# Kernel optimization log

Hardware: AMD Instinct MI355X
Metric: run time of the kernel (lower is better)

## Reference

```python
import jax, jax.numpy as jnp
import numpy as np

N_TRIPLES = 100_000    # number of (head, rel, attr) triples
TOTAL_CHARS = 1_600_000  # total characters across all attribute strings (~16/triple)
CHAR_VOCAB = 10_000
N_ENT = 100_000
D = 128                # embedding dim shared by char and entity tables


def setup_inputs() -> dict:
    key = jax.random.key(0)
    k1, k2, k3, k4, k5 = jax.random.split(key, 5)
    char_embeddings = jax.random.normal(k1, (CHAR_VOCAB, D), dtype=jnp.float32)
    entity_embeddings = jax.random.normal(k2, (N_ENT, D), dtype=jnp.float32)
    head_ids = jax.random.randint(k3, (N_TRIPLES,), 0, N_ENT, dtype=jnp.int32)
    char_ids = jax.random.randint(k4, (TOTAL_CHARS,), 0, CHAR_VOCAB, dtype=jnp.int32)
    # sorted segment ids emulate the per-triple ragged grouping (offsets form)
    segment_ids = jnp.sort(jax.random.randint(k5, (TOTAL_CHARS,), 0, N_TRIPLES, dtype=jnp.int32))
    return {
        "char_embeddings": char_embeddings,
        "entity_embeddings": entity_embeddings,
        "head_ids": head_ids,
        "char_ids": char_ids,
        "segment_ids": segment_ids,
    }


def reference(char_embeddings, entity_embeddings, head_ids, char_ids, segment_ids):
    n = head_ids.shape[0]
    # ragged embedding-bag: gather char rows, sum within each triple's segment
    t = jax.ops.segment_sum(char_embeddings[char_ids], segment_ids, num_segments=n)  # [N, D]
    h = entity_embeddings[head_ids]  # [N, D]
    # torch.norm with no dim = global Frobenius norm (faithful to original)
    h = h / jnp.linalg.norm(h)
    t = t / jnp.linalg.norm(t)
    return jnp.sum(1.0 - jnp.sum(h * t, axis=1))
```

## Files before the change

### kernel.cpp

```cpp
#include <hip/hip_runtime.h>

#define DIM   128
#define HALF  64
#define CPT   256
#define TAIL  64
#define WPB   4
#define NHID  (CPT + 1)

__global__ __launch_bounds__(256) void fused_kernel(
    const float* __restrict__ char_emb,
    const float* __restrict__ ent,
    const int* __restrict__ head_ids,
    const int* __restrict__ char_ids,
    const int* __restrict__ seg_ids,
    float* __restrict__ pb,
    int total_chars, int n_triples, int hh_per_block)
{
    __shared__ __align__(16) int s_off[WPB][CPT + TAIL];
    __shared__ int s_sid[WPB][CPT + TAIL];
    __shared__ int s_hid[WPB][NHID];
    __shared__ float r_scr[3][WPB];

    const int tid  = threadIdx.x;
    const int lane = tid & 63;
    const int wid  = tid >> 6;
    const int colb = lane << 2;

    float ht = 0.f, tt = 0.f, hh = 0.f;

    const int slice = blockIdx.x & 1;
    const int sco   = slice << 8;
    const int chunk = (blockIdx.x >> 1) * WPB + wid;
    const int start = chunk * CPT;
    const int len   = min(CPT, total_chars - start);
    const int sl    = min(CPT + TAIL, total_chars - start);
    const char* cb  = (const char*)char_emb;
    const float* ee = ent + slice * HALF + lane;

    for (int c = lane; c < sl; c += 64) {
        s_off[wid][c] = (char_ids[start + c] << 9) + sco;
        s_sid[wid][c] = seg_ids[start + c];
    }

    unsigned long long mk[4] = {0ull, 0ull, 0ull, 0ull};
    int nb = 0;
    if (len == CPT) {
#pragma unroll
        for (int grp = 0; grp < 4; ++grp) {
            const int c = start + grp * 64 + lane;
            const int s1 = seg_ids[c];
            const int s0 = (c > 0) ? seg_ids[c - 1] : s1;
            const bool bnd = (c == 0) || (s1 != s0);
            const unsigned long long m = __ballot(bnd);
            if (bnd) {
                const int ord = nb + __builtin_amdgcn_mbcnt_hi(
                    (unsigned)(m >> 32),
                    __builtin_amdgcn_mbcnt_lo((unsigned)m, 0));
                s_hid[wid][ord] = head_ids[s0];
            }
            mk[grp] = m;
            nb += __popcll(m);
        }
        if (lane == 0)
            s_hid[wid][nb] = head_ids[seg_ids[start + CPT - 1]];
    }
    __syncthreads();

    if (len == CPT) {
        const int fin = seg_ids[start + CPT - 1];
        float acc = 0.f;
        bool live = false;
        int f = 0;
        const int h0 = s_hid[wid][0];
        const int h1 = s_hid[wid][min(1, nb)];
        int hidn     = s_hid[wid][min(2, nb)];
        float hv  = ee[(size_t)(unsigned)h0 * DIM];
        float hvn = ee[(size_t)(unsigned)h1 * DIM];
        float vA[16], vB[16];

#define PF(BUF, B) { \
    _Pragma("unroll") \
    for (int q = 0; q < 4; ++q) { \
        const int4 o4 = *(const int4*)&s_off[wid][(B) * 16 + q * 4]; \
        BUF[q * 4 + 0] = *(const float*)(cb + (size_t)(unsigned)(o4.x + colb)); \
        BUF[q * 4 + 1] = *(const float*)(cb + (size_t)(unsigned)(o4.y + colb)); \
        BUF[q * 4 + 2] = *(const float*)(cb + (size_t)(unsigned)(o4.z + colb)); \
        BUF[q * 4 + 3] = *(const float*)(cb + (size_t)(unsigned)(o4.w + colb)); \
    } }

#define CS(BUF, B) { \
    _Pragma("unroll") \
    for (int j = 0; j < 16; ++j) { \
        if (mk[(B) >> 2] & (1ull << (((B) & 3) * 16 + j))) {   \
            if (live) { ht = fmaf(hv, acc, ht); tt = fmaf(acc, acc, tt); } \
            live = true; acc = 0.f; \
            hv = hvn;                                     \
            hvn = ee[(size_t)(unsigned)hidn * DIM]; \
            ++f; \
            hidn = s_hid[wid][min(f + 2, nb)]; \
        } \
        acc += BUF[j]; \
    } }

        PF(vA, 0)
#pragma unroll
        for (int B = 0; B < 16; ++B) {
            if (B + 1 < 16) { if (B & 1) { PF(vA, B + 1) } else { PF(vB, B + 1) } }
            if (B & 1) { CS(vB, B) } else { CS(vA, B) }
        }
#undef PF
#undef CS

        if (live) {
            int e = CPT;
            bool ended = false;
            while (e < sl) {
                const int idx = e + lane;
                const bool differ = (idx < sl) && (s_sid[wid][idx] != fin);
                const unsigned long long bm = __ballot(differ);
                const int run = bm ? (__ffsll((long long)bm) - 1)
                                   : min(64, sl - e);
                for (int j = 0; j < run; j += 4) {
                    const int mm2 = min(4, run - j);
                    float vv[4];
#pragma unroll
                    for (int k = 0; k < 4; ++k) {
                        if (k < mm2)
                            vv[k] = *(const float*)(cb +
                                (size_t)(unsigned)(s_off[wid][e + j + k] + colb));
                    }
                    for (int k = 0; k < mm2; ++k) acc += vv[k];
                }
                e += run;
                if (bm) { ended = true; break; }
            }
            if (!ended && start + sl < total_chars) {
                int gg = start + sl;
                while (gg < total_chars && seg_ids[gg] == fin) {
                    acc += *(const float*)(cb +
                        (size_t)(unsigned)((char_ids[gg] << 9) + sco + colb));
                    ++gg;
                }
            }
            ht = fmaf(hv, acc, ht);
            tt = fmaf(acc, acc, tt);
        }
    } else if (len > 0) {
        const float* cembF = char_emb + slice * HALF + lane;
        int p = 0;
        if (start > 0) {
            const int prev = seg_ids[start - 1];
            while (p < len && seg_ids[start + p] == prev) ++p;
        }
        if (p < len) {
            int cur = seg_ids[start + p];
            float acc = 0.f;
            float hv = ee[(size_t)(unsigned)head_ids[cur] * DIM];
            for (int c = p; c < len; ++c) {
                const int sid = seg_ids[start + c];
                if (sid != cur) {
                    ht += hv * acc; tt += acc * acc;
                    acc = 0.f; cur = sid;
                    hv = ee[(size_t)(unsigned)head_ids[cur] * DIM];
                }
                acc += cembF[(size_t)(unsigned)char_ids[start + c] * DIM];
            }
            int gg = start + len;
            while (gg < total_chars && seg_ids[gg] == cur) {
                acc += cembF[(size_t)(unsigned)char_ids[gg] * DIM];
                ++gg;
            }
            ht += hv * acc; tt += acc * acc;
        }
    }

    {
        const float4* e4 = (const float4*)ent;
        const long base = (long)blockIdx.x * hh_per_block * 32;
        const long lim  = (long)n_triples * 32;
        for (int s = tid; s < hh_per_block * 32; s += 256) {
            const long f2 = base + s;
            if (f2 < lim) {
                const int row = (int)(f2 >> 5);
                const int hid = head_ids[row];
                const float4 v = e4[(size_t)hid * 32 + (int)(f2 & 31)];
                hh += v.x * v.x + v.y * v.y + v.z * v.z + v.w * v.w;
            }
        }
    }

#pragma unroll
    for (int off = 32; off > 0; off >>= 1) {
        ht += __shfl_down(ht, off);
        tt += __shfl_down(tt, off);
        hh += __shfl_down(hh, off);
    }
    if (lane == 0) { r_scr[0][wid] = ht; r_scr[1][wid] = tt; r_scr[2][wid] = hh; }
    __syncthreads();
    if (tid == 0) {
        float a = 0.f, b = 0.f, c = 0.f;
#pragma unroll
        for (int w = 0; w < WPB; ++w) {
            a += r_scr[0][w]; b += r_scr[1][w]; c += r_scr[2][w];
        }
        pb[blockIdx.x * 3 + 0] = a;
        pb[blockIdx.x * 3 + 1] = b;
        pb[blockIdx.x * 3 + 2] = c;
    }
}

__global__ __launch_bounds__(256) void reduce_kernel(
    const float* __restrict__ pb, int nb, float* __restrict__ out,
    int n_triples)
{
    double ht = 0.0, tt = 0.0, hh = 0.0;
    for (int i = threadIdx.x; i < nb; i += 256) {
        ht += (double)pb[i * 3 + 0];
        tt += (double)pb[i * 3 + 1];
        hh += (double)pb[i * 3 + 2];
    }
#pragma unroll
    for (int off = 32; off > 0; off >>= 1) {
        ht += __shfl_down(ht, off);
        tt += __shfl_down(tt, off);
        hh += __shfl_down(hh, off);
    }
    __shared__ double sd[3][4];
    const int wid = threadIdx.x >> 6;
    if ((threadIdx.x & 63) == 0) { sd[0][wid] = ht; sd[1][wid] = tt; sd[2][wid] = hh; }
    __syncthreads();
    if (threadIdx.x == 0) {
        double a = 0.0, b = 0.0, c = 0.0;
        for (int w = 0; w < 4; ++w) { a += sd[0][w]; b += sd[1][w]; c += sd[2][w]; }
        out[0] = (float)((double)n_triples - a / sqrt(c * b));
    }
}

extern "C" void kernel_launch(void* const* d_in, const int* in_sizes, int n_in,
                              void* d_out, int out_size, void* d_ws, size_t ws_size,
                              hipStream_t stream)
{
    const float* char_emb = (const float*)d_in[0];
    const float* ent_emb  = (const float*)d_in[1];
    const int* head_ids   = (const int*)d_in[2];
    const int* char_ids   = (const int*)d_in[3];
    const int* seg_ids    = (const int*)d_in[4];
    const int n_triples   = in_sizes[2];
    const int total_chars = in_sizes[3];

    const int n_chunks = (total_chars + CPT - 1) / CPT;
    const int bps = (n_chunks + WPB - 1) / WPB;
    const int nsb = 2 * bps;
    const int hhpb = (n_triples + nsb - 1) / nsb;

    float* pb = (float*)d_ws;

    fused_kernel<<<nsb, 256, 0, stream>>>(char_emb, ent_emb, head_ids,
                                          char_ids, seg_ids, pb,
                                          total_chars, n_triples, hhpb);
    reduce_kernel<<<1, 256, 0, stream>>>(pb, nsb, (float*)d_out, n_triples);
}
```

Before: 184.5 us.

## Defer head-embedding gathers via LDS ring of segment sums and batch them

Segment partial sums are stored into a per-wave LDS ring instead of being combined with the head embedding inside the hot char-accumulation loop. The head-embedding gathers then run afterwards in batches of eight, so their latency overlaps instead of sitting on the critical path. Boundary detection now uses a shuffle instead of a second global load, and the tail offsets and segment ids are no longer staged in LDS but read from global memory. LDS use per block goes up with the ring, which may lower occupancy, and segments beyond the ring size still take the old serial path.

```diff
diff --git a/kernel.cpp b/kernel.cpp
--- a/kernel.cpp
+++ b/kernel.cpp
@@ -5,6 +5,7 @@
 #define CPT   256
 #define TAIL  64
 #define WPB   4
+#define NSEG  22
 #define NHID  (CPT + 1)
 
 __global__ __launch_bounds__(256) void fused_kernel(
@@ -16,9 +17,9 @@
     float* __restrict__ pb,
     int total_chars, int n_triples, int hh_per_block)
 {
-    __shared__ __align__(16) int s_off[WPB][CPT + TAIL];
-    __shared__ int s_sid[WPB][CPT + TAIL];
+    __shared__ __align__(16) int s_off[WPB][CPT];
     __shared__ int s_hid[WPB][NHID];
+    __shared__ float s_ring[WPB][NSEG * 64];
     __shared__ float r_scr[3][WPB];
 
     const int tid  = threadIdx.x;
@@ -37,26 +38,24 @@
     const char* cb  = (const char*)char_emb;
     const float* ee = ent + slice * HALF + lane;
 
-    for (int c = lane; c < sl; c += 64) {
-        s_off[wid][c] = (char_ids[start + c] << 9) + sco;
-        s_sid[wid][c] = seg_ids[start + c];
-    }
-
     unsigned long long mk[4] = {0ull, 0ull, 0ull, 0ull};
     int nb = 0;
     if (len == CPT) {
+        for (int c = lane; c < CPT; c += 64)
+            s_off[wid][c] = (char_ids[start + c] << 9) + sco;
 #pragma unroll
         for (int grp = 0; grp < 4; ++grp) {
             const int c = start + grp * 64 + lane;
             const int s1 = seg_ids[c];
-            const int s0 = (c > 0) ? seg_ids[c - 1] : s1;
-            const bool bnd = (c == 0) || (s1 != s0);
+            int sp = __shfl_up(s1, 1);
+            if (lane == 0) sp = (c > 0) ? seg_ids[c - 1] : s1;
+            const bool bnd = ((grp == 0) && (lane == 0)) || (s1 != sp);
             const unsigned long long m = __ballot(bnd);
             if (bnd) {
                 const int ord = nb + __builtin_amdgcn_mbcnt_hi(
                     (unsigned)(m >> 32),
                     __builtin_amdgcn_mbcnt_lo((unsigned)m, 0));
-                s_hid[wid][ord] = head_ids[s0];
+                s_hid[wid][ord] = (c > 0) ? head_ids[sp] : 0;
             }
             mk[grp] = m;
             nb += __popcll(m);
@@ -68,14 +67,9 @@
 
     if (len == CPT) {
         const int fin = seg_ids[start + CPT - 1];
+        float* ring = &s_ring[wid][0];
         float acc = 0.f;
-        bool live = false;
         int f = 0;
-        const int h0 = s_hid[wid][0];
-        const int h1 = s_hid[wid][min(1, nb)];
-        int hidn     = s_hid[wid][min(2, nb)];
-        float hv  = ee[(size_t)(unsigned)h0 * DIM];
-        float hvn = ee[(size_t)(unsigned)h1 * DIM];
         float vA[16], vB[16];
 
 #define PF(BUF, B) { \
@@ -92,12 +86,14 @@
     _Pragma("unroll") \
     for (int j = 0; j < 16; ++j) { \
         if (mk[(B) >> 2] & (1ull << (((B) & 3) * 16 + j))) {   \
-            if (live) { ht = fmaf(hv, acc, ht); tt = fmaf(acc, acc, tt); } \
-            live = true; acc = 0.f; \
-            hv = hvn;                                     \
-            hvn = ee[(size_t)(unsigned)hidn * DIM]; \
-            ++f; \
-            hidn = s_hid[wid][min(f + 2, nb)]; \
+            if (f < NSEG) { \
+                ring[f * 64 + lane] = acc;           \
+            } else {                                  \
+                const int hid = s_hid[wid][f]; \
+                const float hv = ee[(size_t)(unsigned)hid * DIM]; \
+                ht = fmaf(hv, acc, ht); tt = fmaf(acc, acc, tt); \
+            } \
+            ++f; acc = 0.f; \
         } \
         acc += BUF[j]; \
     } }
@@ -111,12 +107,12 @@
 #undef PF
 #undef CS
 
-        if (live) {
+        {
             int e = CPT;
             bool ended = false;
             while (e < sl) {
                 const int idx = e + lane;
-                const bool differ = (idx < sl) && (s_sid[wid][idx] != fin);
+                const bool differ = (idx < sl) && (seg_ids[start + idx] != fin);
                 const unsigned long long bm = __ballot(differ);
                 const int run = bm ? (__ffsll((long long)bm) - 1)
                                    : min(64, sl - e);
@@ -126,8 +122,8 @@
 #pragma unroll
                     for (int k = 0; k < 4; ++k) {
                         if (k < mm2)
-                            vv[k] = *(const float*)(cb +
-                                (size_t)(unsigned)(s_off[wid][e + j + k] + colb));
+                            vv[k] = *(const float*)(cb + (size_t)(unsigned)(
+                                (char_ids[start + e + j + k] << 9) + sco + colb));
                     }
                     for (int k = 0; k < mm2; ++k) acc += vv[k];
                 }
@@ -137,13 +133,36 @@
             if (!ended && start + sl < total_chars) {
                 int gg = start + sl;
                 while (gg < total_chars && seg_ids[gg] == fin) {
-                    acc += *(const float*)(cb +
-                        (size_t)(unsigned)((char_ids[gg] << 9) + sco + colb));
+                    acc += *(const float*)(cb + (size_t)(unsigned)(
+                        (char_ids[gg] << 9) + sco + colb));
                     ++gg;
                 }
             }
-            ht = fmaf(hv, acc, ht);
-            tt = fmaf(acc, acc, tt);
+        }
+        if (nb < NSEG) {
+            ring[nb * 64 + lane] = acc;
+        } else {
+            const int hid = s_hid[wid][nb];
+            const float hv = ee[(size_t)(unsigned)hid * DIM];
+            ht = fmaf(hv, acc, ht); tt = fmaf(acc, acc, tt);
+        }
+
+        const int fe = min(nb, NSEG - 1);
+        for (int b0 = 1; b0 <= fe; b0 += 8) {
+            const int mc = min(8, fe - b0 + 1);
+            float trb[8], hvb[8];
+#pragma unroll
+            for (int q = 0; q < 8; ++q) {
+                if (q < mc) {
+                    trb[q] = ring[(b0 + q) * 64 + lane];
+                    const int hid = s_hid[wid][b0 + q];
+                    hvb[q] = ee[(size_t)(unsigned)hid * DIM];
+                }
+            }
+            for (int q = 0; q < mc; ++q) {
+                ht = fmaf(hvb[q], trb[q], ht);
+                tt = fmaf(trb[q], trb[q], tt);
+            }
         }
     } else if (len > 0) {
         const float* cembF = char_emb + slice * HALF + lane;
```

Result: no change. 186.5 us (+1.1%).
